# Kernel optimization log

Hardware: AMD Instinct MI355X
Metric: run time of the kernel (lower is better)

Reference implementation:

```python
import jax, jax.numpy as jnp
import numpy as np

D1 = 512
D2 = 1024  # = 2*D1 (concat of x1,y1 along channels)
B, S = 4, 2048


def _self_attn(x, Wq, bq, Wk, bk, Wv, bv):
    # Linear layers use torch convention: out = x @ W.T + b
    q = jnp.einsum('bsd,ed->bse', x, Wq) + bq
    k = jnp.einsum('bsd,ed->bse', x, Wk) + bk
    v = jnp.einsum('bsd,ed->bse', x, Wv) + bv
    # NOTE: original module has no 1/sqrt(d) scaling — keep it faithful.
    scores = jnp.einsum('bqe,bke->bqk', q, k)  # [B,S,S]
    attn = jax.nn.softmax(scores, axis=-1)
    return jnp.einsum('bqk,bke->bqe', attn, v)


def setup_inputs() -> dict:
    key = jax.random.key(0)
    ks = jax.random.split(key, 18)
    s1 = 1.0 / np.sqrt(D1)
    s2 = 1.0 / np.sqrt(D2)
    return {
        'x': jax.random.normal(ks[0], (B, S, D1), jnp.float32),
        'y': jax.random.normal(ks[1], (B, S, D1), jnp.float32),
        'sa1_Wq': jax.random.normal(ks[2], (D1, D1), jnp.float32) * s1,
        'sa1_bq': jnp.zeros((D1,), jnp.float32),
        'sa1_Wk': jax.random.normal(ks[3], (D1, D1), jnp.float32) * s1,
        'sa1_bk': jnp.zeros((D1,), jnp.float32),
        'sa1_Wv': jax.random.normal(ks[4], (D1, D1), jnp.float32) * s1,
        'sa1_bv': jnp.zeros((D1,), jnp.float32),
        'sa2_Wq': jax.random.normal(ks[5], (D2, D2), jnp.float32) * s2,
        'sa2_bq': jnp.zeros((D2,), jnp.float32),
        'sa2_Wk': jax.random.normal(ks[6], (D2, D2), jnp.float32) * s2,
        'sa2_bk': jnp.zeros((D2,), jnp.float32),
        'sa2_Wv': jax.random.normal(ks[7], (D2, D2), jnp.float32) * s2,
        'sa2_bv': jnp.zeros((D2,), jnp.float32),
        'weight1': jnp.ones((1,), jnp.float32),
        'weight2': jnp.ones((1,), jnp.float32),
    }


def reference(x, y, sa1_Wq, sa1_bq, sa1_Wk, sa1_bk, sa1_Wv, sa1_bv,
              sa2_Wq, sa2_bq, sa2_Wk, sa2_bk, sa2_Wv, sa2_bv,
              weight1, weight2):
    x1 = _self_attn(x, sa1_Wq, sa1_bq, sa1_Wk, sa1_bk, sa1_Wv, sa1_bv)
    x1 = x1 + y * weight2
    y1 = _self_attn(y, sa1_Wq, sa1_bq, sa1_Wk, sa1_bk, sa1_Wv, sa1_bv)
    y1 = y1 + x * weight1
    temp = jnp.concatenate((x1, y1), axis=2)  # [B,S,2*D1]
    return _self_attn(temp, sa2_Wq, sa2_bq, sa2_Wk, sa2_bk, sa2_Wv, sa2_bv)
```

## Files before the change

kernel.cpp:

```cpp
#include <hip/hip_runtime.h>
#include <hip/hip_bf16.h>
#include <cstdint>
#include <cstddef>


typedef __bf16 bf16;
typedef __attribute__((ext_vector_type(8))) __bf16 bf16x8;
typedef __attribute__((ext_vector_type(4))) __bf16 bf16x4;
typedef __attribute__((ext_vector_type(4))) float f32x4;

__device__ __forceinline__ void gld16(const bf16* g, bf16* s) {
    __builtin_amdgcn_global_load_lds(
        (const __attribute__((address_space(1))) void*)g,
        (__attribute__((address_space(3))) void*)s, 16, 0, 0);
}

#define WAIT_VM8   __builtin_amdgcn_s_waitcnt(8 | (7 << 4) | (0xF << 8))
#define WAIT_VM0   __builtin_amdgcn_s_waitcnt(0 | (7 << 4) | (0xF << 8))
#define WAIT_LGKM0 __builtin_amdgcn_s_waitcnt(0xF | (7 << 4) | (0 << 8) | (3 << 14))

__device__ __forceinline__ int swz(int row, int g) {
    return row * 64 + ((g ^ (row & 7)) << 3);
}

__global__ __launch_bounds__(256) void gemm_split(
    const bf16* __restrict__ A, long lda, long psA, long bsA,
    const bf16* __restrict__ B, long ldb, long psB, long bsB,
    void* __restrict__ C, long ldc, long psC, long bsC, int mode,
    const float* __restrict__ bias,
    const float* __restrict__ resid, long ldr, long bsR,
    const float* __restrict__ scale,
    int K, int split, int nx, int ny)
{
    __shared__ __align__(16) bf16 As[2][128 * 64];
    __shared__ __align__(16) bf16 Bs[2][128 * 64];

    const int t    = threadIdx.x;
    const int wave = t >> 6;
    const int lane = t & 63;
    const int wr   = wave >> 1;
    const int wc   = wave & 1;
    const int r16  = lane & 15;
    const int quad = lane >> 4;

    const int g    = blockIdx.x;
    const int xcd  = g & 7;
    const int tk   = g >> 3;
    const int nst8 = gridDim.x >> 7;
    const int st   = xcd * nst8 + (tk >> 4);
    const int p    = tk & 15;
    const int snx  = nx >> 2, sny = ny >> 2;
    const int spz  = snx * sny;
    const int zz   = st / spz;
    const int rS   = st - zz * spz;
    const int sy   = rS / snx;
    const int sx   = rS - sy * snx;
    const int yb   = sy * 4 + (p >> 2);
    const int xb   = sx * 4 + (p & 3);
    const long z   = zz;

    const long row0 = (long)yb * 128;
    const long col0 = (long)xb * 128;

    const int srow = (lane >> 3);
    const int scol = ((lane & 7) ^ srow) * 8;

    const int ktiles = K >> 6;
    const int T = split * ktiles;

    const bf16* Az = A + z * bsA;
    const bf16* Bz = B + z * bsB;

    auto prefetch = [&](int ti, int buf) {
        const int ph = ti / ktiles;
        const int kt = (ti - ph * ktiles) << 6;
        const bf16* Ab = Az + (ph == 1 ? psA : 0);
        const bf16* Bb = Bz + (ph == 2 ? psB : 0);
#pragma unroll
        for (int p2 = 0; p2 < 4; ++p2) {
            const int chunk = wave * 32 + p2 * 8;
            gld16(Ab + (row0 + chunk + srow) * lda + kt + scol, &As[buf][chunk * 64]);
            gld16(Bb + (col0 + chunk + srow) * ldb + kt + scol, &Bs[buf][chunk * 64]);
        }
    };

    f32x4 acc[4][4];
#pragma unroll
    for (int r = 0; r < 4; ++r)
#pragma unroll
        for (int c = 0; c < 4; ++c)
            acc[r][c] = (f32x4){0.f, 0.f, 0.f, 0.f};

    prefetch(0, 0);
    prefetch(1, 1);
    for (int ti = 0; ti < T; ++ti) {
        const int cur = ti & 1;
        if (ti + 1 < T) WAIT_VM8; else WAIT_VM0;
        __builtin_amdgcn_s_barrier();
        bf16x8 af[2][4], bg[2][4];
#pragma unroll
        for (int kk = 0; kk < 2; ++kk) {
            const int g0 = (kk << 2) + quad;
#pragma unroll
            for (int r = 0; r < 4; ++r)
                af[kk][r] = *reinterpret_cast<const bf16x8*>(&As[cur][swz(wr * 64 + r * 16 + r16, g0)]);
#pragma unroll
            for (int c = 0; c < 4; ++c)
                bg[kk][c] = *reinterpret_cast<const bf16x8*>(&Bs[cur][swz(wc * 64 + c * 16 + r16, g0)]);
        }
        WAIT_LGKM0;
        __builtin_amdgcn_s_barrier();
        if (ti + 2 < T) prefetch(ti + 2, cur);
#pragma unroll
        for (int kk = 0; kk < 2; ++kk)
#pragma unroll
            for (int r = 0; r < 4; ++r)
#pragma unroll
                for (int c = 0; c < 4; ++c)
                    acc[r][c] = __builtin_amdgcn_mfma_f32_16x16x32_bf16(af[kk][r], bg[kk][c], acc[r][c], 0, 0, 0);
    }

    const float scv = resid ? *scale : 0.f;

#pragma unroll
    for (int r = 0; r < 4; ++r) {
#pragma unroll
        for (int c = 0; c < 4; ++c) {
            long gcol = col0 + wc * 64 + c * 16 + r16;
            float bv = bias ? bias[gcol] : 0.f;
#pragma unroll
            for (int i = 0; i < 4; ++i) {
                long grow = row0 + wr * 64 + r * 16 + quad * 4 + i;
                float val = acc[r][c][i] + bv;
                if (mode == 0) {
                    if (resid) val += resid[z * bsR + grow * ldr + gcol] * scv;
                    ((float*)C)[z * bsC + grow * ldc + gcol] = val;
                } else if (mode == 1) {
                    if (resid) val += resid[z * bsR + grow * ldr + gcol] * scv;
                    bf16* Cb = (bf16*)C + z * bsC;
                    bf16 h = (bf16)val;
                    Cb[grow * ldc + gcol] = h;
                    Cb[psC + grow * ldc + gcol] = (bf16)(val - (float)h);
                } else {
                    long b = grow >> 11, s = grow & 2047;
                    bf16* Cb = (bf16*)C + b * bsC;
                    bf16 h = (bf16)val;
                    Cb[gcol * ldc + s] = h;
                    Cb[psC + gcol * ldc + s] = (bf16)(val - (float)h);
                }
            }
        }
    }
}

__global__ __launch_bounds__(512) void gemm256_scores(
    const bf16* __restrict__ A, long lda, long psA, long bsA,
    const bf16* __restrict__ B, long ldb, long psB, long bsB,
    float* __restrict__ C, long ldc, long bsC, int K)
{
    __shared__ __align__(16) bf16 As[2][256 * 64];
    __shared__ __align__(16) bf16 Bs[2][256 * 64];

    const int t    = threadIdx.x;
    const int wave = t >> 6;
    const int lane = t & 63;
    const int wm   = wave >> 2;
    const int wn   = wave & 3;
    const int r16  = lane & 15;
    const int quad = lane >> 4;

    const int g   = blockIdx.x;
    const int idx = (g & 7) * 32 + (g >> 3);
    const int z   = idx >> 6;
    const int t6  = idx & 63;
    const int ty  = t6 >> 3;
    const int tx  = t6 & 7;
    const long row0 = (long)ty * 256;
    const long col0 = (long)tx * 256;

    const int srow = lane >> 3;
    const int scol = ((lane & 7) ^ srow) * 8;

    const int ktiles = K >> 6;
    const int T = 3 * ktiles;

    const bf16* Az = A + (long)z * bsA;
    const bf16* Bz = B + (long)z * bsB;

    auto prefetch = [&](int ti, int buf) {
        const int ph = ti / ktiles;
        const int kt = (ti - ph * ktiles) << 6;
        const bf16* Ab = Az + (ph == 1 ? psA : 0);
        const bf16* Bb = Bz + (ph == 2 ? psB : 0);
#pragma unroll
        for (int p2 = 0; p2 < 4; ++p2) {
            const int chunk = wave * 32 + p2 * 8;
            gld16(Ab + (row0 + chunk + srow) * lda + kt + scol, &As[buf][chunk * 64]);
            gld16(Bb + (col0 + chunk + srow) * ldb + kt + scol, &Bs[buf][chunk * 64]);
        }
    };

    f32x4 acc[8][4];
#pragma unroll
    for (int r = 0; r < 8; ++r)
#pragma unroll
        for (int c = 0; c < 4; ++c)
            acc[r][c] = (f32x4){0.f, 0.f, 0.f, 0.f};

    bf16x8 af[4][2];
    bf16x8 bg[2][2][2];

    prefetch(0, 0);
    prefetch(1, 1);
    for (int ti = 0; ti < T; ++ti) {
        const int cur = ti & 1;
        if (ti + 1 < T) WAIT_VM8; else WAIT_VM0;
        __builtin_amdgcn_s_barrier();

#pragma unroll
        for (int kk = 0; kk < 2; ++kk) {
            const int g0 = (kk << 2) + quad;
#pragma unroll
            for (int r = 0; r < 4; ++r)
                af[r][kk] = *reinterpret_cast<const bf16x8*>(
                    &As[cur][swz(wm * 128 + r * 16 + r16, g0)]);
#pragma unroll
            for (int c = 0; c < 2; ++c)
                bg[0][c][kk] = *reinterpret_cast<const bf16x8*>(
                    &Bs[cur][swz(wn * 64 + c * 16 + r16, g0)]);
        }
        __builtin_amdgcn_s_barrier();
        WAIT_LGKM0;
        __builtin_amdgcn_s_setprio(1);
#pragma unroll
        for (int kk = 0; kk < 2; ++kk)
#pragma unroll
            for (int r = 0; r < 4; ++r)
#pragma unroll
                for (int c = 0; c < 2; ++c)
                    acc[r][c] = __builtin_amdgcn_mfma_f32_16x16x32_bf16(
                        af[r][kk], bg[0][c][kk], acc[r][c], 0, 0, 0);
        __builtin_amdgcn_s_setprio(0);
        __builtin_amdgcn_s_barrier();

#pragma unroll
        for (int kk = 0; kk < 2; ++kk) {
            const int g0 = (kk << 2) + quad;
#pragma unroll
            for (int c = 0; c < 2; ++c)
                bg[1][c][kk] = *reinterpret_cast<const bf16x8*>(
                    &Bs[cur][swz(wn * 64 + (2 + c) * 16 + r16, g0)]);
        }
        __builtin_amdgcn_s_barrier();
        WAIT_LGKM0;
        __builtin_amdgcn_s_setprio(1);
#pragma unroll
        for (int kk = 0; kk < 2; ++kk)
#pragma unroll
            for (int r = 0; r < 4; ++r)
#pragma unroll
                for (int c = 0; c < 2; ++c)
                    acc[r][2 + c] = __builtin_amdgcn_mfma_f32_16x16x32_bf16(
                        af[r][kk], bg[1][c][kk], acc[r][2 + c], 0, 0, 0);
        __builtin_amdgcn_s_setprio(0);
        __builtin_amdgcn_s_barrier();

#pragma unroll
        for (int kk = 0; kk < 2; ++kk) {
            const int g0 = (kk << 2) + quad;
#pragma unroll
            for (int r = 0; r < 4; ++r)
                af[r][kk] = *reinterpret_cast<const bf16x8*>(
                    &As[cur][swz(wm * 128 + (4 + r) * 16 + r16, g0)]);
        }
        __builtin_amdgcn_s_barrier();
        WAIT_LGKM0;
        __builtin_amdgcn_s_setprio(1);
#pragma unroll
        for (int kk = 0; kk < 2; ++kk)
#pragma unroll
            for (int r = 0; r < 4; ++r)
#pragma unroll
                for (int c = 0; c < 2; ++c)
                    acc[4 + r][c] = __builtin_amdgcn_mfma_f32_16x16x32_bf16(
                        af[r][kk], bg[0][c][kk], acc[4 + r][c], 0, 0, 0);
        __builtin_amdgcn_s_setprio(0);
        __builtin_amdgcn_s_barrier();
        if (ti + 2 < T) prefetch(ti + 2, cur);

        __builtin_amdgcn_s_setprio(1);
#pragma unroll
        for (int kk = 0; kk < 2; ++kk)
#pragma unroll
            for (int r = 0; r < 4; ++r)
#pragma unroll
                for (int c = 0; c < 2; ++c)
                    acc[4 + r][2 + c] = __builtin_amdgcn_mfma_f32_16x16x32_bf16(
                        af[r][kk], bg[1][c][kk], acc[4 + r][2 + c], 0, 0, 0);
        __builtin_amdgcn_s_setprio(0);
    }

#pragma unroll
    for (int r = 0; r < 8; ++r) {
#pragma unroll
        for (int c = 0; c < 4; ++c) {
            const long gcol = col0 + wn * 64 + c * 16 + r16;
#pragma unroll
            for (int i = 0; i < 4; ++i) {
                const long grow = row0 + wm * 128 + r * 16 + quad * 4 + i;
                C[(long)z * bsC + grow * ldc + gcol] = acc[r][c][i];
            }
        }
    }
}

__global__ __launch_bounds__(256) void softmax_planes(float* __restrict__ S)
{
    __shared__ float redm[4], reds[4];
    float* srow = S + (long)blockIdx.x * 2048;
    const int t = threadIdx.x;
    const int lane = t & 63;
    const int wave = t >> 6;

    f32x4 v0 = *reinterpret_cast<const f32x4*>(srow + t * 4);
    f32x4 v1 = *reinterpret_cast<const f32x4*>(srow + 1024 + t * 4);

    float m = v0[0];
#pragma unroll
    for (int i = 1; i < 4; ++i) m = fmaxf(m, v0[i]);
#pragma unroll
    for (int i = 0; i < 4; ++i) m = fmaxf(m, v1[i]);
#pragma unroll
    for (int off = 32; off > 0; off >>= 1) m = fmaxf(m, __shfl_xor(m, off));
    if (lane == 0) redm[wave] = m;
    __syncthreads();
    m = fmaxf(fmaxf(redm[0], redm[1]), fmaxf(redm[2], redm[3]));

    float s = 0.f;
#pragma unroll
    for (int i = 0; i < 4; ++i) { v0[i] = __expf(v0[i] - m); s += v0[i]; }
#pragma unroll
    for (int i = 0; i < 4; ++i) { v1[i] = __expf(v1[i] - m); s += v1[i]; }
#pragma unroll
    for (int off = 32; off > 0; off >>= 1) s += __shfl_xor(s, off);
    if (lane == 0) reds[wave] = s;
    __syncthreads();
    s = reds[0] + reds[1] + reds[2] + reds[3];
    float inv = 1.f / s;

    bf16x4 h0, h1, l0, l1;
#pragma unroll
    for (int i = 0; i < 4; ++i) {
        float a = v0[i] * inv, b = v1[i] * inv;
        h0[i] = (bf16)a; l0[i] = (bf16)(a - (float)h0[i]);
        h1[i] = (bf16)b; l1[i] = (bf16)(b - (float)h1[i]);
    }
    bf16* ph = (bf16*)srow;
    *reinterpret_cast<bf16x4*>(ph + t * 4) = h0;
    *reinterpret_cast<bf16x4*>(ph + 1024 + t * 4) = h1;
    *reinterpret_cast<bf16x4*>(ph + 2048 + t * 4) = l0;
    *reinterpret_cast<bf16x4*>(ph + 3072 + t * 4) = l1;
}

__global__ __launch_bounds__(256) void split_f32(
    const float* __restrict__ in, bf16* __restrict__ hi, long n)
{
    long i = ((long)blockIdx.x * 256 + threadIdx.x) * 4;
    f32x4 v = *reinterpret_cast<const f32x4*>(in + i);
    bf16x4 h, l;
#pragma unroll
    for (int j = 0; j < 4; ++j) {
        h[j] = (bf16)v[j];
        l[j] = (bf16)(v[j] - (float)h[j]);
    }
    *reinterpret_cast<bf16x4*>(hi + i) = h;
    *reinterpret_cast<bf16x4*>(hi + n + i) = l;
}

extern "C" void kernel_launch(void* const* d_in, const int* in_sizes, int n_in,
                              void* d_out, int out_size, void* d_ws, size_t ws_size,
                              hipStream_t stream)
{
    const float* x   = (const float*)d_in[0];
    const float* y   = (const float*)d_in[1];
    const float* Wq1 = (const float*)d_in[2];
    const float* bq1 = (const float*)d_in[3];
    const float* Wk1 = (const float*)d_in[4];
    const float* bk1 = (const float*)d_in[5];
    const float* Wv1 = (const float*)d_in[6];
    const float* bv1 = (const float*)d_in[7];
    const float* Wq2 = (const float*)d_in[8];
    const float* bq2 = (const float*)d_in[9];
    const float* Wk2 = (const float*)d_in[10];
    const float* bk2 = (const float*)d_in[11];
    const float* Wv2 = (const float*)d_in[12];
    const float* bv2 = (const float*)d_in[13];
    const float* w1  = (const float*)d_in[14];
    const float* w2  = (const float*)d_in[15];
    float* out = (float*)d_out;

    const size_t MB = 1ull << 20;
    char* ws = (char*)d_ws;
    const long S = 2048, M4 = 8192, E1 = 512, E2 = 1024;
    const long W1ps = E1 * E1, W2ps = E2 * E2;

    const int cfg = (ws_size >= 207 * MB) ? 2 : 0;

    bf16 *Wq1p, *Wk1p, *Wv1p, *Wq2p, *Wk2p, *Wv2p, *temp, *qb, *kb, *vt;
    float* Sc;
    bf16* xp = (bf16*)d_out;
    bf16* yp = xp + 2 * M4 * E1;
    if (cfg == 2) {
        Wq1p = (bf16*)(ws + 0 * MB);  Wk1p = (bf16*)(ws + 1 * MB);  Wv1p = (bf16*)(ws + 2 * MB);
        Wq2p = (bf16*)(ws + 3 * MB);  Wk2p = (bf16*)(ws + 7 * MB);  Wv2p = (bf16*)(ws + 11 * MB);
        temp = (bf16*)(ws + 15 * MB);
        qb   = (bf16*)(ws + 47 * MB);
        kb   = (bf16*)(ws + 79 * MB);
        vt   = (bf16*)(ws + 111 * MB);
        Sc   = (float*)(ws + 143 * MB);
    } else {
        Wq1p = (bf16*)(ws + 0 * MB);  Wk1p = (bf16*)(ws + 1 * MB);  Wv1p = (bf16*)(ws + 2 * MB);
        temp = (bf16*)(ws + 3 * MB);
        qb   = (bf16*)(ws + 35 * MB);
        kb   = (bf16*)(ws + 43 * MB);
        vt   = (bf16*)(ws + 51 * MB);
        Sc   = (float*)(ws + 59 * MB);
        Wq2p = (bf16*)d_out;
        Wk2p = Wq2p + 2 * W2ps;
        Wv2p = Wk2p + 2 * W2ps;
    }

    auto gemm = [&](const bf16* A, long lda, long psA, long bsA,
                    const bf16* B, long ldb, long psB, long bsB,
                    void* C, long ldc, long psC, long bsC, int mode,
                    const float* bias, const float* resid, long ldr, long bsR,
                    const float* scale, int M, int N, int K, int split, int gz) {
        int nx = N / 128, ny = M / 128;
        dim3 g((unsigned)(nx * ny * gz));
        gemm_split<<<g, dim3(256), 0, stream>>>(
            A, lda, psA, bsA, B, ldb, psB, bsB, C, ldc, psC, bsC, mode,
            bias, resid, ldr, bsR, scale, K, split, nx, ny);
    };
    auto scores256 = [&](const bf16* A, long lda, long psA, long bsA,
                         const bf16* B, long ldb, long psB, long bsB,
                         float* C, int K) {
        gemm256_scores<<<dim3(256), dim3(512), 0, stream>>>(
            A, lda, psA, bsA, B, ldb, psB, bsB, C, S, S * S, K);
    };
    auto conv = [&](const float* in, bf16* planes, long n) {
        split_f32<<<dim3((unsigned)(n / 1024)), dim3(256), 0, stream>>>(in, planes, n);
    };

    conv(x, xp, M4 * E1);
    conv(y, yp, M4 * E1);
    conv(Wq1, Wq1p, W1ps); conv(Wk1, Wk1p, W1ps); conv(Wv1, Wv1p, W1ps);
    if (cfg == 2) { conv(Wq2, Wq2p, W2ps); conv(Wk2, Wk2p, W2ps); conv(Wv2, Wv2p, W2ps); }

    auto stage1 = [&](const bf16* sp, const float* resid, const float* scale, long colOff) {
        if (cfg == 2) {
            gemm(sp, E1, M4 * E1, 0, Wq1p, E1, W1ps, 0, qb, E1, M4 * E1, 0, 1,
                 bq1, nullptr, 0, 0, nullptr, 8192, 512, 512, 3, 1);
            gemm(sp, E1, M4 * E1, 0, Wk1p, E1, W1ps, 0, kb, E1, M4 * E1, 0, 1,
                 bk1, nullptr, 0, 0, nullptr, 8192, 512, 512, 3, 1);
            gemm(sp, E1, M4 * E1, 0, Wv1p, E1, W1ps, 0, vt, S, E1 * S, 2 * E1 * S, 2,
                 bv1, nullptr, 0, 0, nullptr, 8192, 512, 512, 3, 1);
            scores256(qb, E1, M4 * E1, S * E1, kb, E1, M4 * E1, S * E1, Sc, 512);
            softmax_planes<<<dim3(8192), dim3(256), 0, stream>>>(Sc);
            gemm((const bf16*)Sc, 4096, 2048, S * 4096, vt, S, E1 * S, 2 * E1 * S,
                 temp + colOff, 1024, M4 * 1024, S * 1024, 1,
                 nullptr, resid, E1, S * E1, scale, 2048, 512, 2048, 3, 4);
        } else {
            for (int b = 0; b < 4; ++b) {
                const bf16* sb = sp + (long)b * S * E1;
                gemm(sb, E1, M4 * E1, 0, Wq1p, E1, W1ps, 0, qb, E1, S * E1, 0, 1,
                     bq1, nullptr, 0, 0, nullptr, 2048, 512, 512, 3, 1);
                gemm(sb, E1, M4 * E1, 0, Wk1p, E1, W1ps, 0, kb, E1, S * E1, 0, 1,
                     bk1, nullptr, 0, 0, nullptr, 2048, 512, 512, 3, 1);
                gemm(sb, E1, M4 * E1, 0, Wv1p, E1, W1ps, 0, vt, S, E1 * S, 0, 2,
                     bv1, nullptr, 0, 0, nullptr, 2048, 512, 512, 3, 1);
                gemm(qb, E1, S * E1, 0, kb, E1, S * E1, 0, Sc, S, 0, 0, 0,
                     nullptr, nullptr, 0, 0, nullptr, 2048, 2048, 512, 3, 1);
                softmax_planes<<<dim3(2048), dim3(256), 0, stream>>>(Sc);
                gemm((const bf16*)Sc, 4096, 2048, 0, vt, S, E1 * S, 0,
                     temp + colOff + (long)b * S * 1024, 1024, M4 * 1024, 0, 1,
                     nullptr, resid + (long)b * S * E1, E1, 0, scale, 2048, 512, 2048, 3, 1);
            }
        }
    };

    stage1(xp, y, w2, 0);
    stage1(yp, x, w1, 512);

    if (cfg == 0) { conv(Wq2, Wq2p, W2ps); conv(Wk2, Wk2p, W2ps); conv(Wv2, Wv2p, W2ps); }

    if (cfg == 2) {
        gemm(temp, E2, M4 * E2, 0, Wq2p, E2, W2ps, 0, qb, E2, M4 * E2, 0, 1,
             bq2, nullptr, 0, 0, nullptr, 8192, 1024, 1024, 3, 1);
        gemm(temp, E2, M4 * E2, 0, Wk2p, E2, W2ps, 0, kb, E2, M4 * E2, 0, 1,
             bk2, nullptr, 0, 0, nullptr, 8192, 1024, 1024, 3, 1);
        gemm(temp, E2, M4 * E2, 0, Wv2p, E2, W2ps, 0, vt, S, E2 * S, 2 * E2 * S, 2,
             bv2, nullptr, 0, 0, nullptr, 8192, 1024, 1024, 1, 1);
        scores256(qb, E2, M4 * E2, S * E2, kb, E2, M4 * E2, S * E2, Sc, 1024);
        softmax_planes<<<dim3(8192), dim3(256), 0, stream>>>(Sc);
        gemm((const bf16*)Sc, 4096, 2048, S * 4096, vt, S, E2 * S, 2 * E2 * S,
             out, E2, 0, S * E2, 0, nullptr, nullptr, 0, 0, nullptr,
             2048, 1024, 2048, 1, 4);
    } else {
        for (int b = 0; b < 4; ++b) {
            const bf16* tb = temp + (long)b * S * E2;
            gemm(tb, E2, M4 * E2, 0, Wq2p, E2, W2ps, 0, qb, E2, S * E2, 0, 1,
                 bq2, nullptr, 0, 0, nullptr, 2048, 1024, 1024, 3, 1);
            gemm(tb, E2, M4 * E2, 0, Wk2p, E2, W2ps, 0, kb, E2, S * E2, 0, 1,
                 bk2, nullptr, 0, 0, nullptr, 2048, 1024, 1024, 3, 1);
            gemm(tb, E2, M4 * E2, 0, Wv2p, E2, W2ps, 0, vt, S, E2 * S, 0, 2,
                 bv2, nullptr, 0, 0, nullptr, 2048, 1024, 1024, 1, 1);
            gemm(qb, E2, S * E2, 0, kb, E2, S * E2, 0, Sc, S, 0, 0, 0,
                 nullptr, nullptr, 0, 0, nullptr, 2048, 2048, 1024, 3, 1);
            softmax_planes<<<dim3(2048), dim3(256), 0, stream>>>(Sc);
            gemm((const bf16*)Sc, 4096, 2048, 0, vt, S, E2 * S, 0,
                 out + (long)b * S * E2, E2, 0, 0, 0, nullptr, nullptr, 0, 0, nullptr,
                 2048, 1024, 2048, 1, 1);
        }
    }

    (void)in_sizes; (void)n_in; (void)out_size;
}
```

Before: 1.007 ms.

## Issue all LDS fragment loads up front and cut GEMM loop barriers

The GEMM main loop now issues every LDS read for the tile (both A halves and both B halves) at the start of each k-tile, then runs the MFMAs. There is a single waitcnt plus barrier before the next global prefetch, replacing four load/barrier/compute phases. This removes most intra-loop barriers and lets the LDS reads overlap with the first MFMAs. The cost is more live fragment registers, which could lower occupancy or cause spills.

```diff
diff --git a/kernel.cpp b/kernel.cpp
--- a/kernel.cpp
+++ b/kernel.cpp
@@ -207,9 +207,6 @@
         for (int c = 0; c < 4; ++c)
             acc[r][c] = (f32x4){0.f, 0.f, 0.f, 0.f};
 
-    bf16x8 af[4][2];
-    bf16x8 bg[2][2][2];
-
     prefetch(0, 0);
     prefetch(1, 1);
     for (int ti = 0; ti < T; ++ti) {
@@ -217,32 +214,23 @@
         if (ti + 1 < T) WAIT_VM8; else WAIT_VM0;
         __builtin_amdgcn_s_barrier();
 
+        bf16x8 afA[4][2], afB[4][2], bg[2][2][2];
 #pragma unroll
         for (int kk = 0; kk < 2; ++kk) {
             const int g0 = (kk << 2) + quad;
 #pragma unroll
             for (int r = 0; r < 4; ++r)
-                af[r][kk] = *reinterpret_cast<const bf16x8*>(
+                afA[r][kk] = *reinterpret_cast<const bf16x8*>(
                     &As[cur][swz(wm * 128 + r * 16 + r16, g0)]);
+        }
+#pragma unroll
+        for (int kk = 0; kk < 2; ++kk) {
+            const int g0 = (kk << 2) + quad;
 #pragma unroll
             for (int c = 0; c < 2; ++c)
                 bg[0][c][kk] = *reinterpret_cast<const bf16x8*>(
                     &Bs[cur][swz(wn * 64 + c * 16 + r16, g0)]);
         }
-        __builtin_amdgcn_s_barrier();
-        WAIT_LGKM0;
-        __builtin_amdgcn_s_setprio(1);
-#pragma unroll
-        for (int kk = 0; kk < 2; ++kk)
-#pragma unroll
-            for (int r = 0; r < 4; ++r)
-#pragma unroll
-                for (int c = 0; c < 2; ++c)
-                    acc[r][c] = __builtin_amdgcn_mfma_f32_16x16x32_bf16(
-                        af[r][kk], bg[0][c][kk], acc[r][c], 0, 0, 0);
-        __builtin_amdgcn_s_setprio(0);
-        __builtin_amdgcn_s_barrier();
-
 #pragma unroll
         for (int kk = 0; kk < 2; ++kk) {
             const int g0 = (kk << 2) + quad;
@@ -251,9 +239,24 @@
                 bg[1][c][kk] = *reinterpret_cast<const bf16x8*>(
                     &Bs[cur][swz(wn * 64 + (2 + c) * 16 + r16, g0)]);
         }
-        __builtin_amdgcn_s_barrier();
-        WAIT_LGKM0;
+#pragma unroll
+        for (int kk = 0; kk < 2; ++kk) {
+            const int g0 = (kk << 2) + quad;
+#pragma unroll
+            for (int r = 0; r < 4; ++r)
+                afB[r][kk] = *reinterpret_cast<const bf16x8*>(
+                    &As[cur][swz(wm * 128 + (4 + r) * 16 + r16, g0)]);
+        }
+
         __builtin_amdgcn_s_setprio(1);
+#pragma unroll
+        for (int kk = 0; kk < 2; ++kk)
+#pragma unroll
+            for (int r = 0; r < 4; ++r)
+#pragma unroll
+                for (int c = 0; c < 2; ++c)
+                    acc[r][c] = __builtin_amdgcn_mfma_f32_16x16x32_bf16(
+                        afA[r][kk], bg[0][c][kk], acc[r][c], 0, 0, 0);
 #pragma unroll
         for (int kk = 0; kk < 2; ++kk)
 #pragma unroll
@@ -261,20 +264,14 @@
 #pragma unroll
                 for (int c = 0; c < 2; ++c)
                     acc[r][2 + c] = __builtin_amdgcn_mfma_f32_16x16x32_bf16(
-                        af[r][kk], bg[1][c][kk], acc[r][2 + c], 0, 0, 0);
+                        afA[r][kk], bg[1][c][kk], acc[r][2 + c], 0, 0, 0);
         __builtin_amdgcn_s_setprio(0);
+
+        __builtin_amdgcn_sched_barrier(0);
+        WAIT_LGKM0;
         __builtin_amdgcn_s_barrier();
-
-#pragma unroll
-        for (int kk = 0; kk < 2; ++kk) {
-            const int g0 = (kk << 2) + quad;
-#pragma unroll
-            for (int r = 0; r < 4; ++r)
-                af[r][kk] = *reinterpret_cast<const bf16x8*>(
-                    &As[cur][swz(wm * 128 + (4 + r) * 16 + r16, g0)]);
-        }
-        __builtin_amdgcn_s_barrier();
-        WAIT_LGKM0;
+        if (ti + 2 < T) prefetch(ti + 2, cur);
+
         __builtin_amdgcn_s_setprio(1);
 #pragma unroll
         for (int kk = 0; kk < 2; ++kk)
@@ -283,12 +280,7 @@
 #pragma unroll
                 for (int c = 0; c < 2; ++c)
                     acc[4 + r][c] = __builtin_amdgcn_mfma_f32_16x16x32_bf16(
-                        af[r][kk], bg[0][c][kk], acc[4 + r][c], 0, 0, 0);
-        __builtin_amdgcn_s_setprio(0);
-        __builtin_amdgcn_s_barrier();
-        if (ti + 2 < T) prefetch(ti + 2, cur);
-
-        __builtin_amdgcn_s_setprio(1);
+                        afB[r][kk], bg[0][c][kk], acc[4 + r][c], 0, 0, 0);
 #pragma unroll
         for (int kk = 0; kk < 2; ++kk)
 #pragma unroll
@@ -296,7 +288,7 @@
 #pragma unroll
                 for (int c = 0; c < 2; ++c)
                     acc[4 + r][2 + c] = __builtin_amdgcn_mfma_f32_16x16x32_bf16(
-                        af[r][kk], bg[1][c][kk], acc[4 + r][2 + c], 0, 0, 0);
+                        afB[r][kk], bg[1][c][kk], acc[4 + r][2 + c], 0, 0, 0);
         __builtin_amdgcn_s_setprio(0);
     }
 
```

Result: faster. 986.5 us (-2.1%).
